# Performance work log

Hardware: AMD Instinct MI355X
Metric: run time of the kernel (lower is better)

The kernel has to match this reference:

```python
import jax, jax.numpy as jnp
import numpy as np

B, L, DM, DH = 8, 2048, 1024, 1024


def setup_inputs() -> dict:
    key = jax.random.key(0)
    ks = jax.random.split(key, 10)
    s_dm = 1.0 / np.sqrt(DM)   # nn.Linear(d_model, *) init bound
    s_dh = 1.0 / np.sqrt(DH)   # nn.Linear(d_hidden, *) init bound
    u = lambda k, shp, s: jax.random.uniform(k, shp, jnp.float32, -s, s)
    return {
        "x": jax.random.normal(ks[0], (B, L, DM), jnp.float32),
        # A scaled by 0.01 so cumprod(exp(delta*A)) stays finite over L=2048
        "A": 0.01 * jax.random.normal(ks[1], (DH,), jnp.float32),
        "Bw": u(ks[2], (DH, DM), s_dm), "Bb": u(ks[3], (DH,), s_dm),
        "Cw": u(ks[4], (DM, DH), s_dh), "Cb": u(ks[5], (DM,), s_dh),
        "Dw": u(ks[6], (DM, DM), s_dm), "Db": u(ks[7], (DM,), s_dm),
        "dw": u(ks[8], (DH, DM), s_dm), "db": u(ks[9], (DH,), s_dm),
    }


def reference(x, A, Bw, Bb, Cw, Cb, Dw, Db, dw, db):
    # x: [B, L, DM]
    delta = jax.nn.softplus(jnp.einsum('bld,hd->blh', x, dw) + db)   # [B,L,DH]
    A_bar = jnp.exp(delta * A)                                        # [B,L,DH]
    B_bar = delta * (jnp.einsum('bld,hd->blh', x, Bw) + Bb)           # [B,L,DH]
    A_cum = jnp.cumprod(A_bar, axis=1)                                # [B,L,DH]
    h = jnp.cumsum(B_bar / A_cum, axis=1) * A_cum                     # [B,L,DH]
    out = jnp.einsum('blh,dh->bld', h, Cw) + Cb \
        + jnp.einsum('bld,ed->ble', x, Dw) + Db                       # [B,L,DM]
    return out
```

## Files before the change

### kernel.cpp

```cpp
#include <hip/hip_runtime.h>
#include <hip/hip_bf16.h>
#include <stdint.h>

#define DMODEL 1024
#define DHID   1024
#define NBATCH 8
#define LSEQ   2048
#define MROWS  (NBATCH * LSEQ)
#define KCAT   2048
#define CH     32
#define NCH    64
#define BH     (NBATCH * DHID)

typedef __attribute__((ext_vector_type(8))) short  short8;
typedef __attribute__((ext_vector_type(8))) __bf16 bf16x8;
typedef __attribute__((ext_vector_type(4))) float  f32x4;

__device__ __forceinline__ unsigned short f2bf(float f) {
  union { float f; unsigned int u; } v; v.f = f;
  unsigned int u = v.u;
  u += 0x7fffu + ((u >> 16) & 1u);
  return (unsigned short)(u >> 16);
}

__device__ __forceinline__ float bf2f(unsigned short s) {
  union { unsigned int u; float f; } v; v.u = ((unsigned int)s) << 16;
  return v.f;
}

__device__ __forceinline__ float softplus_f(float x) {
  return fmaxf(x, 0.f) + log1pf(expf(-fabsf(x)));
}

__device__ __forceinline__ short8 pack8(float4 a, float4 b) {
  short8 o;
  o[0] = (short)f2bf(a.x); o[1] = (short)f2bf(a.y);
  o[2] = (short)f2bf(a.z); o[3] = (short)f2bf(a.w);
  o[4] = (short)f2bf(b.x); o[5] = (short)f2bf(b.y);
  o[6] = (short)f2bf(b.z); o[7] = (short)f2bf(b.w);
  return o;
}

__global__ __launch_bounds__(256)
void cast_all_kernel(const float* __restrict__ x,
                     const float* __restrict__ dw, const float* __restrict__ Bw,
                     const float* __restrict__ Cw, const float* __restrict__ Dw,
                     unsigned short* __restrict__ A2,
                     unsigned short* __restrict__ W1, unsigned short* __restrict__ W2) {
  const size_t MX = (size_t)MROWS * 1024;
  const size_t M1 = (size_t)2048 * 1024;
  size_t i8 = ((size_t)blockIdx.x * 256 + threadIdx.x) * 8;
  if (i8 < MX) {
    size_t row = i8 >> 10; int col = (int)(i8 & 1023);
    const float4* p = (const float4*)(x + i8);
    *(short8*)(A2 + row * (size_t)KCAT + 1024 + col) = pack8(p[0], p[1]);
  } else if (i8 < MX + M1) {
    size_t k = i8 - MX;
    size_t row = k >> 10; int col = (int)(k & 1023);
    size_t h = row >> 1;
    const float* src = (row & 1) ? (Bw + h * 1024 + col) : (dw + h * 1024 + col);
    const float4* p = (const float4*)src;
    *(short8*)(W1 + k) = pack8(p[0], p[1]);
  } else {
    size_t k = i8 - MX - M1;
    size_t d = k >> 11; int c = (int)(k & 2047);
    const float* src = (c < 1024) ? (Cw + d * 1024 + c) : (Dw + d * 1024 + (c - 1024));
    const float4* p = (const float4*)src;
    *(short8*)(W2 + k) = pack8(p[0], p[1]);
  }
}

__device__ __forceinline__ void stage_tile(const unsigned short* g0, int ld,
                                           unsigned short* s0, int t, int lane) {
#pragma unroll
  for (int half = 0; half < 2; ++half) {
    int c = t + half * 256;
    const unsigned short* g = g0 + (size_t)(c >> 2) * ld + (c & 3) * 8;
    unsigned short* s = s0 + ((size_t)(t - lane) + half * 256) * 8;
    __builtin_amdgcn_global_load_lds(
        (const __attribute__((address_space(1))) unsigned int*)g,
        (__attribute__((address_space(3))) unsigned int*)s, 16, 0, 0);
  }
}

__global__ __launch_bounds__(256, 4)
void gemm_bt(const unsigned short* __restrict__ A, int lda,
             const unsigned short* __restrict__ B, int ldb,
             void* __restrict__ Cp, int ldc, int K, int mode,
             const float* __restrict__ bias0, const float* __restrict__ bias1) {
  __shared__ __align__(16) unsigned short As[128 * 32];
  __shared__ __align__(16) unsigned short Bs[128 * 32];
  const int t = threadIdx.x;
  const int lane = t & 63, wave = t >> 6;
  const int quad = lane >> 4, l16 = lane & 15;

  const int Nt = gridDim.x, Mt = gridDim.y;
  int bid = blockIdx.y * Nt + blockIdx.x;
  int xcd = bid & 7;
  int slot = bid >> 3;
  int lm = slot / Nt;
  int ln = slot - lm * Nt;
  const int m0 = (xcd * (Mt >> 3) + lm) * 128;
  const int n0 = ln * 128;

  const int wm = (wave & 1) * 64, wn = (wave >> 1) * 64;

  const unsigned short* Ab = A + (size_t)m0 * lda;
  const unsigned short* Bb = B + (size_t)n0 * ldb;

  f32x4 acc[4][4] = {};

  for (int k0 = 0; k0 < K; k0 += 32) {
    stage_tile(Ab + k0, lda, As, t, lane);
    stage_tile(Bb + k0, ldb, Bs, t, lane);
    __syncthreads();
    short8 af[4], bfr[4];
#pragma unroll
    for (int i = 0; i < 4; ++i)
      af[i] = *(const short8*)(As + ((size_t)(wm + i * 16 + l16)) * 32 + quad * 8);
#pragma unroll
    for (int j = 0; j < 4; ++j)
      bfr[j] = *(const short8*)(Bs + ((size_t)(wn + j * 16 + l16)) * 32 + quad * 8);
#pragma unroll
    for (int i = 0; i < 4; ++i)
#pragma unroll
      for (int j = 0; j < 4; ++j)
        acc[i][j] = __builtin_amdgcn_mfma_f32_16x16x32_bf16(
            __builtin_bit_cast(bf16x8, af[i]),
            __builtin_bit_cast(bf16x8, bfr[j]), acc[i][j], 0, 0, 0);
    __syncthreads();
  }

  if (mode == 0) {
    float* C = (float*)Cp;
#pragma unroll
    for (int i = 0; i < 4; ++i)
#pragma unroll
      for (int j = 0; j < 4; ++j) {
        int n = n0 + wn + j * 16 + l16;
        int mb = m0 + wm + i * 16 + quad * 4;
        float badd = bias0[n] + bias1[n];
#pragma unroll
        for (int r = 0; r < 4; ++r)
          C[(size_t)(mb + r) * ldc + n] = acc[i][j][r] + badd;
      }
  } else {
    unsigned short* G = (unsigned short*)Cp;
    const int even = !(lane & 1);
#pragma unroll
    for (int j = 0; j < 4; ++j) {
      int n = n0 + wn + j * 16 + l16;
      int h = n >> 1;
      float dbh = bias0[h], Bbh = bias1[h];
#pragma unroll
      for (int i = 0; i < 4; ++i) {
        int mb = m0 + wm + i * 16 + quad * 4;
#pragma unroll
        for (int r = 0; r < 4; ++r) {
          float mine = acc[i][j][r];
          float other = __shfl_xor(mine, 1, 64);
          float dpre = even ? mine : other;
          float bpre = even ? other : mine;
          float d = softplus_f(dpre + dbh);
          float bb = d * (bpre + Bbh);
          size_t off = (size_t)(mb + r) * KCAT + h + (even ? 0 : 1024);
          G[off] = f2bf(even ? d : bb);
        }
      }
    }
  }
}

__global__ __launch_bounds__(256)
void scan_carry_kernel(const unsigned short* __restrict__ G1,
                       const float* __restrict__ Av, float2* __restrict__ carr) {
  int t = blockIdx.x * 256 + threadIdx.x;
  int ho = t & 127, chunk = (t >> 7) & (NCH - 1), b = t >> 13;
  int h0 = ho << 3;
  float4 A0 = *(const float4*)(Av + h0), A1 = *(const float4*)(Av + h0 + 4);
  float Ah[8] = {A0.x, A0.y, A0.z, A0.w, A1.x, A1.y, A1.z, A1.w};
  const unsigned short* base = G1 + ((size_t)(b * LSEQ + chunk * CH)) * KCAT + h0;
  float hs[8] = {}, sd[8] = {};
#pragma unroll 4
  for (int l = 0; l < CH; ++l) {
    short8 dp = *(const short8*)(base + (size_t)l * KCAT);
    short8 bp = *(const short8*)(base + (size_t)l * KCAT + 1024);
#pragma unroll
    for (int j = 0; j < 8; ++j) {
      float d = bf2f((unsigned short)dp[j]);
      sd[j] += d;
      float a = __expf(d * Ah[j]);
      hs[j] = fmaf(a, hs[j], bf2f((unsigned short)bp[j]));
    }
  }
  float2* cb = carr + (size_t)chunk * BH + b * 1024 + h0;
#pragma unroll
  for (int j = 0; j < 8; ++j)
    cb[j] = make_float2(__expf(Ah[j] * sd[j]), hs[j]);
}

__global__ __launch_bounds__(256)
void scan_comb_kernel(const float2* __restrict__ carr, float* __restrict__ Hc) {
  int t = blockIdx.x * 256 + threadIdx.x;
  float H = 0.f;
#pragma unroll
  for (int c = 0; c < NCH; ++c) {
    float2 ah = carr[(size_t)c * BH + t];
    Hc[(size_t)c * BH + t] = H;
    H = fmaf(ah.x, H, ah.y);
  }
}

__global__ __launch_bounds__(256)
void scan_final_kernel(const unsigned short* __restrict__ G1,
                       const float* __restrict__ Av, const float* __restrict__ Hc,
                       unsigned short* __restrict__ A2) {
  int t = blockIdx.x * 256 + threadIdx.x;
  int ho = t & 127, chunk = (t >> 7) & (NCH - 1), b = t >> 13;
  int h0 = ho << 3;
  float4 A0 = *(const float4*)(Av + h0), A1 = *(const float4*)(Av + h0 + 4);
  float Ah[8] = {A0.x, A0.y, A0.z, A0.w, A1.x, A1.y, A1.z, A1.w};
  const unsigned short* base = G1 + ((size_t)(b * LSEQ + chunk * CH)) * KCAT + h0;
  unsigned short* obase = A2 + ((size_t)(b * LSEQ + chunk * CH)) * KCAT + h0;
  const float* hb = Hc + (size_t)chunk * BH + b * 1024 + h0;
  float hs[8];
#pragma unroll
  for (int j = 0; j < 8; ++j) hs[j] = hb[j];
#pragma unroll 4
  for (int l = 0; l < CH; ++l) {
    short8 dp = *(const short8*)(base + (size_t)l * KCAT);
    short8 bp = *(const short8*)(base + (size_t)l * KCAT + 1024);
    short8 o;
#pragma unroll
    for (int j = 0; j < 8; ++j) {
      float d = bf2f((unsigned short)dp[j]);
      float a = __expf(d * Ah[j]);
      hs[j] = fmaf(a, hs[j], bf2f((unsigned short)bp[j]));
      o[j] = (short)f2bf(hs[j]);
    }
    *(short8*)(obase + (size_t)l * KCAT) = o;
  }
}

extern "C" void kernel_launch(void* const* d_in, const int* in_sizes, int n_in,
                              void* d_out, int out_size, void* d_ws, size_t ws_size,
                              hipStream_t stream) {
  const float* x  = (const float*)d_in[0];
  const float* Av = (const float*)d_in[1];
  const float* Bw = (const float*)d_in[2];
  const float* Bb = (const float*)d_in[3];
  const float* Cw = (const float*)d_in[4];
  const float* Cb = (const float*)d_in[5];
  const float* Dw = (const float*)d_in[6];
  const float* Db = (const float*)d_in[7];
  const float* dw = (const float*)d_in[8];
  const float* db = (const float*)d_in[9];
  float* out = (float*)d_out;

  const size_t sz_big = (size_t)MROWS * KCAT * 2;
  const size_t sz_w   = (size_t)2048 * 1024 * 2;
  const size_t sz_hc  = (size_t)NCH * BH * 4;
  const size_t need = 2 * sz_big + 2 * sz_w + sz_hc;
  if (ws_size < need) return;

  char* w = (char*)d_ws;
  unsigned short* A2 = (unsigned short*)w; w += sz_big;
  unsigned short* G1 = (unsigned short*)w; w += sz_big;
  unsigned short* W1 = (unsigned short*)w; w += sz_w;
  unsigned short* W2 = (unsigned short*)w; w += sz_w;
  float* Hc = (float*)w;                   w += sz_hc;
  float2* carr = (float2*)W1;

  const size_t cast_elems = (size_t)MROWS * 1024 + 2 * (size_t)2048 * 1024;
  cast_all_kernel<<<(int)(cast_elems / (256 * 8)), 256, 0, stream>>>(
      x, dw, Bw, Cw, Dw, A2, W1, W2);

  dim3 g1(KCAT / 128, MROWS / 128);
  gemm_bt<<<g1, 256, 0, stream>>>(A2 + 1024, KCAT, W1, 1024, G1, KCAT, 1024, 2,
                                  db, Bb);

  scan_carry_kernel<<<(NBATCH * NCH * 128) / 256, 256, 0, stream>>>(G1, Av, carr);
  scan_comb_kernel<<<BH / 256, 256, 0, stream>>>(carr, Hc);
  scan_final_kernel<<<(NBATCH * NCH * 128) / 256, 256, 0, stream>>>(G1, Av, Hc, A2);

  dim3 g2(DMODEL / 128, MROWS / 128);
  gemm_bt<<<g2, 256, 0, stream>>>(A2, KCAT, W2, KCAT, out, DMODEL, KCAT, 0, Cb, Db);
}
```

Before: 398.3 us.

## Move softplus and bias epilogue from GEMM into scan carry pass

The first GEMM now writes raw bf16 projections with a plain epilogue, and the weight layout is changed from interleaved dw/Bw rows to two contiguous blocks. The softplus, bias adds and delta*B product move into scan_carry_kernel, which computes them and writes the results back in place for scan_final to read. This removes the lane shuffles and scattered stores from the GEMM epilogue and simplifies the weight cast. In exchange the scan carry pass does extra transcendental work and a read-modify-write of the whole G1 buffer.

```diff
diff --git a/kernel.cpp b/kernel.cpp
--- a/kernel.cpp
+++ b/kernel.cpp
@@ -48,21 +48,19 @@
                      unsigned short* __restrict__ A2,
                      unsigned short* __restrict__ W1, unsigned short* __restrict__ W2) {
   const size_t MX = (size_t)MROWS * 1024;
-  const size_t M1 = (size_t)2048 * 1024;
+  const size_t M1 = (size_t)1024 * 1024;
   size_t i8 = ((size_t)blockIdx.x * 256 + threadIdx.x) * 8;
   if (i8 < MX) {
     size_t row = i8 >> 10; int col = (int)(i8 & 1023);
     const float4* p = (const float4*)(x + i8);
     *(short8*)(A2 + row * (size_t)KCAT + 1024 + col) = pack8(p[0], p[1]);
-  } else if (i8 < MX + M1) {
+  } else if (i8 < MX + 2 * M1) {
     size_t k = i8 - MX;
-    size_t row = k >> 10; int col = (int)(k & 1023);
-    size_t h = row >> 1;
-    const float* src = (row & 1) ? (Bw + h * 1024 + col) : (dw + h * 1024 + col);
+    const float* src = (k < M1) ? (dw + k) : (Bw + k - M1);
     const float4* p = (const float4*)src;
     *(short8*)(W1 + k) = pack8(p[0], p[1]);
   } else {
-    size_t k = i8 - MX - M1;
+    size_t k = i8 - MX - 2 * M1;
     size_t d = k >> 11; int c = (int)(k & 2047);
     const float* src = (c < 1024) ? (Cw + d * 1024 + c) : (Dw + d * 1024 + (c - 1024));
     const float4* p = (const float4*)src;
@@ -145,53 +143,54 @@
           C[(size_t)(mb + r) * ldc + n] = acc[i][j][r] + badd;
       }
   } else {
-    unsigned short* G = (unsigned short*)Cp;
-    const int even = !(lane & 1);
-#pragma unroll
-    for (int j = 0; j < 4; ++j) {
-      int n = n0 + wn + j * 16 + l16;
-      int h = n >> 1;
-      float dbh = bias0[h], Bbh = bias1[h];
-#pragma unroll
-      for (int i = 0; i < 4; ++i) {
+    unsigned short* C16 = (unsigned short*)Cp;
+#pragma unroll
+    for (int i = 0; i < 4; ++i)
+#pragma unroll
+      for (int j = 0; j < 4; ++j) {
+        int n = n0 + wn + j * 16 + l16;
         int mb = m0 + wm + i * 16 + quad * 4;
 #pragma unroll
-        for (int r = 0; r < 4; ++r) {
-          float mine = acc[i][j][r];
-          float other = __shfl_xor(mine, 1, 64);
-          float dpre = even ? mine : other;
-          float bpre = even ? other : mine;
-          float d = softplus_f(dpre + dbh);
-          float bb = d * (bpre + Bbh);
-          size_t off = (size_t)(mb + r) * KCAT + h + (even ? 0 : 1024);
-          G[off] = f2bf(even ? d : bb);
-        }
+        for (int r = 0; r < 4; ++r)
+          C16[(size_t)(mb + r) * ldc + n] = f2bf(acc[i][j][r]);
       }
-    }
-  }
-}
-
-__global__ __launch_bounds__(256)
-void scan_carry_kernel(const unsigned short* __restrict__ G1,
-                       const float* __restrict__ Av, float2* __restrict__ carr) {
+  }
+}
+
+__global__ __launch_bounds__(256)
+void scan_carry_kernel(unsigned short* __restrict__ G1,
+                       const float* __restrict__ Av, const float* __restrict__ Bbv,
+                       const float* __restrict__ dbv, float2* __restrict__ carr) {
   int t = blockIdx.x * 256 + threadIdx.x;
   int ho = t & 127, chunk = (t >> 7) & (NCH - 1), b = t >> 13;
   int h0 = ho << 3;
-  float4 A0 = *(const float4*)(Av + h0), A1 = *(const float4*)(Av + h0 + 4);
-  float Ah[8] = {A0.x, A0.y, A0.z, A0.w, A1.x, A1.y, A1.z, A1.w};
-  const unsigned short* base = G1 + ((size_t)(b * LSEQ + chunk * CH)) * KCAT + h0;
+  float4 A0 = *(const float4*)(Av + h0),  A1 = *(const float4*)(Av + h0 + 4);
+  float4 B0 = *(const float4*)(Bbv + h0), B1 = *(const float4*)(Bbv + h0 + 4);
+  float4 D0 = *(const float4*)(dbv + h0), D1 = *(const float4*)(dbv + h0 + 4);
+  float Ah[8]  = {A0.x, A0.y, A0.z, A0.w, A1.x, A1.y, A1.z, A1.w};
+  float Bbh[8] = {B0.x, B0.y, B0.z, B0.w, B1.x, B1.y, B1.z, B1.w};
+  float dbh[8] = {D0.x, D0.y, D0.z, D0.w, D1.x, D1.y, D1.z, D1.w};
+  unsigned short* base = G1 + ((size_t)(b * LSEQ + chunk * CH)) * KCAT + h0;
   float hs[8] = {}, sd[8] = {};
-#pragma unroll 4
+#pragma unroll 2
   for (int l = 0; l < CH; ++l) {
     short8 dp = *(const short8*)(base + (size_t)l * KCAT);
     short8 bp = *(const short8*)(base + (size_t)l * KCAT + 1024);
+    short8 dq, bq;
 #pragma unroll
     for (int j = 0; j < 8; ++j) {
-      float d = bf2f((unsigned short)dp[j]);
-      sd[j] += d;
-      float a = __expf(d * Ah[j]);
-      hs[j] = fmaf(a, hs[j], bf2f((unsigned short)bp[j]));
+      float d = softplus_f(bf2f((unsigned short)dp[j]) + dbh[j]);
+      unsigned short dr = f2bf(d);
+      float drf = bf2f(dr);
+      float bb = drf * (bf2f((unsigned short)bp[j]) + Bbh[j]);
+      unsigned short br = f2bf(bb);
+      sd[j] += drf;
+      float a = __expf(drf * Ah[j]);
+      hs[j] = fmaf(a, hs[j], bf2f(br));
+      dq[j] = (short)dr; bq[j] = (short)br;
     }
+    *(short8*)(base + (size_t)l * KCAT) = dq;
+    *(short8*)(base + (size_t)l * KCAT + 1024) = bq;
   }
   float2* cb = carr + (size_t)chunk * BH + b * 1024 + h0;
 #pragma unroll
@@ -276,10 +275,10 @@
       x, dw, Bw, Cw, Dw, A2, W1, W2);
 
   dim3 g1(KCAT / 128, MROWS / 128);
-  gemm_bt<<<g1, 256, 0, stream>>>(A2 + 1024, KCAT, W1, 1024, G1, KCAT, 1024, 2,
-                                  db, Bb);
-
-  scan_carry_kernel<<<(NBATCH * NCH * 128) / 256, 256, 0, stream>>>(G1, Av, carr);
+  gemm_bt<<<g1, 256, 0, stream>>>(A2 + 1024, KCAT, W1, 1024, G1, KCAT, 1024, 1,
+                                  nullptr, nullptr);
+
+  scan_carry_kernel<<<(NBATCH * NCH * 128) / 256, 256, 0, stream>>>(G1, Av, Bb, db, carr);
   scan_comb_kernel<<<BH / 256, 256, 0, stream>>>(carr, Hc);
   scan_final_kernel<<<(NBATCH * NCH * 128) / 256, 256, 0, stream>>>(G1, Av, Hc, A2);
 
```

Measured after the change: 391.0 us. About the same (-1.8%).
